# Kernel tuning notes

Hardware: AMD Instinct MI355X
Metric: run time of the kernel (lower is better)

The kernel has to match this reference:

```python
import jax, jax.numpy as jnp
import numpy as np

WINDOW = 512
STEP = 256
N_FREQ = 256
EPS = 1e-8


def setup_inputs() -> dict:
    key = jax.random.key(0)
    k1, k2, k3 = jax.random.split(key, 3)
    audio = jax.random.normal(k1, (512, 32768), dtype=jnp.float32)
    basis_real = jax.random.normal(k2, (N_FREQ, WINDOW), dtype=jnp.float32)
    basis_imag = jax.random.normal(k3, (N_FREQ, WINDOW), dtype=jnp.float32)
    return {"audio": audio, "basis_real": basis_real, "basis_imag": basis_imag}


def reference(audio, basis_real, basis_imag):
    # --- framing (windowed_audio): strided unfold -> [B, n_frames, WINDOW] ---
    n_samples = audio.shape[-1]
    n_frames = (n_samples - WINDOW) // STEP + 1  # 127 for 32768 samples
    idx = jnp.arange(n_frames)[:, None] * STEP + jnp.arange(WINDOW)[None, :]
    windowed = audio[:, idx]  # [B, F, W]

    # --- per-frame L2 normalization ---
    norms = jnp.linalg.norm(windowed, axis=-1, keepdims=True)  # [B, F, 1]
    wn = windowed / (norms + EPS)

    # --- basis normalization by complex L2 norm over window dim ---
    bnorm = jnp.sqrt(jnp.sum(basis_real * basis_real + basis_imag * basis_imag,
                             axis=-1, keepdims=True))  # [K, 1]
    br = basis_real / (bnorm + EPS)
    bi = basis_imag / (bnorm + EPS)

    # --- projection: windowed @ basis.T, real and imag parts ---
    real = jnp.einsum('bfw,kw->bfk', wn, br)  # [B, F, K]
    imag = jnp.einsum('bfw,kw->bfk', wn, bi)  # [B, F, K]
    return norms, real, imag
```

## Files before the change

### kernel.cpp

```cpp
#include <hip/hip_runtime.h>

#define WINDOW   512
#define STEPSZ   256
#define NFRAMES  127
#define NSAMP    32768
#define NBATCH   512
#define NFREQ    256
#define BM       64
#define SAMP_TILE 16640
#define NPS      65

typedef __attribute__((ext_vector_type(8)))  short short8;
typedef __attribute__((ext_vector_type(16))) float f32x16;
typedef __attribute__((ext_vector_type(4)))  float f4;

#define SWZ(byt) ((byt) ^ ((((byt) >> 9) & 7) << 4))

static __device__ __forceinline__ short f2bf(float x) {
    union { float f; unsigned u; } v; v.f = x;
    unsigned r = (v.u + 0x7fffu + ((v.u >> 16) & 1u)) >> 16;
    return (short)r;
}

__global__ __launch_bounds__(256) void prep_kernel(const float* __restrict__ br,
                                                   const float* __restrict__ bi,
                                                   short* __restrict__ Bf) {
    const int lane = threadIdx.x & 63;
    const int wid  = threadIdx.x >> 6;
    const int n    = blockIdx.x * 4 + wid;
    const float* pr = br + (size_t)n * WINDOW + lane * 8;
    const float* pi = bi + (size_t)n * WINDOW + lane * 8;
    f4 r0 = *(const f4*)pr;
    f4 r1 = *(const f4*)(pr + 4);
    f4 i0 = *(const f4*)pi;
    f4 i1 = *(const f4*)(pi + 4);
    float ss = 0.f;
#pragma unroll
    for (int j = 0; j < 4; ++j)
        ss += r0[j]*r0[j] + r1[j]*r1[j] + i0[j]*i0[j] + i1[j]*i1[j];
#pragma unroll
    for (int d = 1; d < 64; d <<= 1) ss += __shfl_xor(ss, d, 64);
    const float inv = 1.0f / (sqrtf(ss) + 1e-8f);
    short8 hr, hi;
#pragma unroll
    for (int j = 0; j < 4; ++j) {
        hr[j]     = f2bf(r0[j] * inv);
        hr[j + 4] = f2bf(r1[j] * inv);
        hi[j]     = f2bf(i0[j] * inv);
        hi[j + 4] = f2bf(i1[j] * inv);
    }
    const int ks  = lane >> 1, kg2 = lane & 1;
    const int nsR = n >> 5;
    const int nsI = 8 + (n >> 5);
    const int sl  = (n & 31) + 32 * kg2;
    *(short8*)(Bf + ((size_t)(nsR * 32 + ks) * 64 + sl) * 8) = hr;
    *(short8*)(Bf + ((size_t)(nsI * 32 + ks) * 64 + sl) * 8) = hi;
}

__global__ __launch_bounds__(512, 4) void mel_kernel(const float* __restrict__ audio,
                                                     const short* __restrict__ Bf,
                                                     float* __restrict__ out) {
    __shared__ short smp[SAMP_TILE];
    __shared__ float ps[NPS];
    __shared__ float invn[BM];

    const int tid  = threadIdx.x;
    const int lane = tid & 63;
    const int wid  = tid >> 6;

    const int b  = blockIdx.x >> 1;
    const int mh = blockIdx.x & 1;
    const int f0 = mh * BM;

    float* out_norms = out;
    float* out_real  = out + 65024;
    float* out_imag  = out + 65024 + 16646144;

    const float* abase = audio + (size_t)b * NSAMP + f0 * STEPSZ;
    const int smax = NSAMP - f0 * STEPSZ - 8;

    const int rl32 = lane & 31;
    const int kg2  = lane >> 5;
    const int wn   = wid;

    const short* bp0 = Bf + ((size_t)(2 * wn + 0) * 32 * 64 + lane) * 8;
    const short* bp1 = Bf + ((size_t)(2 * wn + 1) * 32 * 64 + lane) * 8;

    short8 bb[3][2];
#pragma unroll
    for (int d = 0; d < 3; ++d) {
        bb[d][0] = *(const short8*)(bp0 + (size_t)d * 512);
        bb[d][1] = *(const short8*)(bp1 + (size_t)d * 512);
    }

#pragma unroll
    for (int it = 0; it < 5; ++it) {
        const int sl = it * 4096 + tid * 8;
        float ss = 0.f;
        if (sl < SAMP_TILE) {
            const int slc = sl < smax ? sl : smax;
            f4 v0 = *(const f4*)(abase + slc);
            f4 v1 = *(const f4*)(abase + slc + 4);
            short8 h;
#pragma unroll
            for (int q = 0; q < 4; ++q) {
                ss += v0[q]*v0[q] + v1[q]*v1[q];
                h[q]     = f2bf(v0[q]);
                h[q + 4] = f2bf(v1[q]);
            }
            const int byt = sl * 2;
            *(short8*)((char*)smp + SWZ(byt)) = h;
        }
        ss += __shfl_xor(ss, 1, 64);
        ss += __shfl_xor(ss, 2, 64);
        ss += __shfl_xor(ss, 4, 64);
        ss += __shfl_xor(ss, 8, 64);
        ss += __shfl_xor(ss, 16, 64);
        const int chunk = (it * 4096 + tid * 8) >> 8;
        if ((tid & 31) == 0 && chunk < NPS) ps[chunk] = ss;
    }
    __syncthreads();

    if (tid < BM) {
        const float nrm = sqrtf(ps[tid] + ps[tid + 1]);
        const int fr = f0 + tid;
        if (fr < NFRAMES) out_norms[b * NFRAMES + fr] = nrm;
        invn[tid] = 1.0f / (nrm + 1e-8f);
    }

    const int rb0 = (0 * 32 + rl32) * 512 + kg2 * 16;
    const int rb1 = (1 * 32 + rl32) * 512 + kg2 * 16;
    const int X0  = (rl32 & 7) << 4;
    const int X1  = ((rl32 + 1) & 7) << 4;
    const char* sb = (const char*)smp;

    f32x16 acc[2][2];
    acc[0][0] = (f32x16)0.f; acc[0][1] = (f32x16)0.f;
    acc[1][0] = (f32x16)0.f; acc[1][1] = (f32x16)0.f;

#pragma unroll
    for (int ks = 0; ks < 32; ++ks) {
        const int X  = (ks < 16) ? X0 : X1;
        const int kb = ks * 32;
        short8 a0 = *(const short8*)(sb + ((rb0 + kb) ^ X));
        short8 a1 = *(const short8*)(sb + ((rb1 + kb) ^ X));
        const int cur = ks % 3;
        short8 cb0 = bb[cur][0];
        short8 cb1 = bb[cur][1];
        if (ks < 29) {
            bb[cur][0] = *(const short8*)(bp0 + (size_t)(ks + 3) * 512);
            bb[cur][1] = *(const short8*)(bp1 + (size_t)(ks + 3) * 512);
        }
        acc[0][0] = __builtin_amdgcn_mfma_f32_32x32x16_bf16(a0, cb0, acc[0][0], 0, 0, 0);
        acc[1][0] = __builtin_amdgcn_mfma_f32_32x32x16_bf16(a1, cb0, acc[1][0], 0, 0, 0);
        acc[0][1] = __builtin_amdgcn_mfma_f32_32x32x16_bf16(a0, cb1, acc[0][1], 0, 0, 0);
        acc[1][1] = __builtin_amdgcn_mfma_f32_32x32x16_bf16(a1, cb1, acc[1][1], 0, 0, 0);
    }
    __syncthreads();

#pragma unroll
    for (int mi = 0; mi < 2; ++mi) {
#pragma unroll
        for (int s = 0; s < 2; ++s) {
            const int n = (2 * wn + s) * 32 + rl32;
            float* dst = (n < NFREQ) ? out_real : out_imag;
            const int kcol = n & (NFREQ - 1);
            const int rbase = mi * 32 + 4 * kg2;
#pragma unroll
            for (int r = 0; r < 16; ++r) {
                const int rr = rbase + (r & 3) + 8 * (r >> 2);
                const int fr = f0 + rr;
                if (fr < NFRAMES)
                    dst[((size_t)b * NFRAMES + fr) * NFREQ + kcol] = acc[mi][s][r] * invn[rr];
            }
        }
    }
}

extern "C" void kernel_launch(void* const* d_in, const int* in_sizes, int n_in,
                              void* d_out, int out_size, void* d_ws, size_t ws_size,
                              hipStream_t stream) {
    const float* audio = (const float*)d_in[0];
    const float* br    = (const float*)d_in[1];
    const float* bi    = (const float*)d_in[2];
    float* out = (float*)d_out;
    short* Bf  = (short*)d_ws;

    prep_kernel<<<64, 256, 0, stream>>>(br, bi, Bf);
    mel_kernel<<<NBATCH * 2, 512, 0, stream>>>(audio, Bf, out);
}
```

Before: 63.16 us.

## Process both frame halves per block with double-buffered LDS staging overlapped with MFMA

Each block now handles a whole batch row, covering both 64-frame halves instead of one. While the MFMA loop runs on the first half, the audio for the second half is loaded, converted to bf16 and written into a second LDS buffer. The basis prefetch changes from a 3-deep ring to an even/odd 2-deep scheme. This hides global-load latency behind compute, but it halves the grid to 512 blocks and doubles LDS per block, which can cut occupancy and parallelism.

```diff
diff --git a/kernel.cpp b/kernel.cpp
--- a/kernel.cpp
+++ b/kernel.cpp
@@ -57,121 +57,185 @@
     *(short8*)(Bf + ((size_t)(nsI * 32 + ks) * 64 + sl) * 8) = hi;
 }
 
+#define STAGE_ISSUE(IT)                                                   \
+    if (!last) {                                                          \
+        const int sl = (IT) * 4096 + tid * 8;                             \
+        if (sl < SAMP_TILE) {                                             \
+            const int slc = sl < smax_n ? sl : smax_n;                    \
+            sv0 = *(const f4*)(abase_n + slc);                            \
+            sv1 = *(const f4*)(abase_n + slc + 4);                        \
+        }                                                                 \
+    }
+
+#define STAGE_USE(IT)                                                     \
+    if (!last) {                                                          \
+        const int sl = (IT) * 4096 + tid * 8;                             \
+        float ss = 0.f;                                                   \
+        if (sl < SAMP_TILE) {                                             \
+            short8 h;                                                     \
+            _Pragma("unroll")                                             \
+            for (int q = 0; q < 4; ++q) {                                 \
+                ss += sv0[q]*sv0[q] + sv1[q]*sv1[q];                      \
+                h[q]     = f2bf(sv0[q]);                                  \
+                h[q + 4] = f2bf(sv1[q]);                                  \
+            }                                                             \
+            *(short8*)((char*)smp[s1] + SWZ(sl * 2)) = h;                 \
+        }                                                                 \
+        ss += __shfl_xor(ss, 1, 64);                                      \
+        ss += __shfl_xor(ss, 2, 64);                                      \
+        ss += __shfl_xor(ss, 4, 64);                                      \
+        ss += __shfl_xor(ss, 8, 64);                                      \
+        ss += __shfl_xor(ss, 16, 64);                                     \
+        const int chunk = ((IT) * 4096 + tid * 8) >> 8;                   \
+        if ((tid & 31) == 0 && chunk < NPS) ps[s1][chunk] = ss;           \
+    }
+
 __global__ __launch_bounds__(512, 4) void mel_kernel(const float* __restrict__ audio,
                                                      const short* __restrict__ Bf,
                                                      float* __restrict__ out) {
-    __shared__ short smp[SAMP_TILE];
-    __shared__ float ps[NPS];
-    __shared__ float invn[BM];
+    __shared__ short smp[2][SAMP_TILE];
+    __shared__ float ps[2][NPS];
+    __shared__ float invn[2][BM];
 
     const int tid  = threadIdx.x;
     const int lane = tid & 63;
     const int wid  = tid >> 6;
 
-    const int b  = blockIdx.x >> 1;
-    const int mh = blockIdx.x & 1;
-    const int f0 = mh * BM;
+    const int b = blockIdx.x;
 
     float* out_norms = out;
     float* out_real  = out + 65024;
     float* out_imag  = out + 65024 + 16646144;
 
-    const float* abase = audio + (size_t)b * NSAMP + f0 * STEPSZ;
-    const int smax = NSAMP - f0 * STEPSZ - 8;
-
     const int rl32 = lane & 31;
     const int kg2  = lane >> 5;
     const int wn   = wid;
 
     const short* bp0 = Bf + ((size_t)(2 * wn + 0) * 32 * 64 + lane) * 8;
     const short* bp1 = Bf + ((size_t)(2 * wn + 1) * 32 * 64 + lane) * 8;
-
-    short8 bb[3][2];
-#pragma unroll
-    for (int d = 0; d < 3; ++d) {
-        bb[d][0] = *(const short8*)(bp0 + (size_t)d * 512);
-        bb[d][1] = *(const short8*)(bp1 + (size_t)d * 512);
-    }
-
-#pragma unroll
-    for (int it = 0; it < 5; ++it) {
-        const int sl = it * 4096 + tid * 8;
-        float ss = 0.f;
-        if (sl < SAMP_TILE) {
-            const int slc = sl < smax ? sl : smax;
-            f4 v0 = *(const f4*)(abase + slc);
-            f4 v1 = *(const f4*)(abase + slc + 4);
-            short8 h;
-#pragma unroll
-            for (int q = 0; q < 4; ++q) {
-                ss += v0[q]*v0[q] + v1[q]*v1[q];
-                h[q]     = f2bf(v0[q]);
-                h[q + 4] = f2bf(v1[q]);
-            }
-            const int byt = sl * 2;
-            *(short8*)((char*)smp + SWZ(byt)) = h;
-        }
-        ss += __shfl_xor(ss, 1, 64);
-        ss += __shfl_xor(ss, 2, 64);
-        ss += __shfl_xor(ss, 4, 64);
-        ss += __shfl_xor(ss, 8, 64);
-        ss += __shfl_xor(ss, 16, 64);
-        const int chunk = (it * 4096 + tid * 8) >> 8;
-        if ((tid & 31) == 0 && chunk < NPS) ps[chunk] = ss;
-    }
-    __syncthreads();
-
-    if (tid < BM) {
-        const float nrm = sqrtf(ps[tid] + ps[tid + 1]);
-        const int fr = f0 + tid;
-        if (fr < NFRAMES) out_norms[b * NFRAMES + fr] = nrm;
-        invn[tid] = 1.0f / (nrm + 1e-8f);
-    }
 
     const int rb0 = (0 * 32 + rl32) * 512 + kg2 * 16;
     const int rb1 = (1 * 32 + rl32) * 512 + kg2 * 16;
     const int X0  = (rl32 & 7) << 4;
     const int X1  = ((rl32 + 1) & 7) << 4;
-    const char* sb = (const char*)smp;
-
-    f32x16 acc[2][2];
-    acc[0][0] = (f32x16)0.f; acc[0][1] = (f32x16)0.f;
-    acc[1][0] = (f32x16)0.f; acc[1][1] = (f32x16)0.f;
-
-#pragma unroll
-    for (int ks = 0; ks < 32; ++ks) {
-        const int X  = (ks < 16) ? X0 : X1;
-        const int kb = ks * 32;
-        short8 a0 = *(const short8*)(sb + ((rb0 + kb) ^ X));
-        short8 a1 = *(const short8*)(sb + ((rb1 + kb) ^ X));
-        const int cur = ks % 3;
-        short8 cb0 = bb[cur][0];
-        short8 cb1 = bb[cur][1];
-        if (ks < 29) {
-            bb[cur][0] = *(const short8*)(bp0 + (size_t)(ks + 3) * 512);
-            bb[cur][1] = *(const short8*)(bp1 + (size_t)(ks + 3) * 512);
-        }
-        acc[0][0] = __builtin_amdgcn_mfma_f32_32x32x16_bf16(a0, cb0, acc[0][0], 0, 0, 0);
-        acc[1][0] = __builtin_amdgcn_mfma_f32_32x32x16_bf16(a1, cb0, acc[1][0], 0, 0, 0);
-        acc[0][1] = __builtin_amdgcn_mfma_f32_32x32x16_bf16(a0, cb1, acc[0][1], 0, 0, 0);
-        acc[1][1] = __builtin_amdgcn_mfma_f32_32x32x16_bf16(a1, cb1, acc[1][1], 0, 0, 0);
-    }
-    __syncthreads();
-
-#pragma unroll
-    for (int mi = 0; mi < 2; ++mi) {
-#pragma unroll
-        for (int s = 0; s < 2; ++s) {
-            const int n = (2 * wn + s) * 32 + rl32;
-            float* dst = (n < NFREQ) ? out_real : out_imag;
-            const int kcol = n & (NFREQ - 1);
-            const int rbase = mi * 32 + 4 * kg2;
-#pragma unroll
-            for (int r = 0; r < 16; ++r) {
-                const int rr = rbase + (r & 3) + 8 * (r >> 2);
-                const int fr = f0 + rr;
-                if (fr < NFRAMES)
-                    dst[((size_t)b * NFRAMES + fr) * NFREQ + kcol] = acc[mi][s][r] * invn[rr];
+
+    {
+        const float* abase = audio + (size_t)b * NSAMP;
+        const int smax = NSAMP - 8;
+#pragma unroll
+        for (int it = 0; it < 5; ++it) {
+            const int sl = it * 4096 + tid * 8;
+            float ss = 0.f;
+            if (sl < SAMP_TILE) {
+                const int slc = sl < smax ? sl : smax;
+                f4 v0 = *(const f4*)(abase + slc);
+                f4 v1 = *(const f4*)(abase + slc + 4);
+                short8 h;
+#pragma unroll
+                for (int q = 0; q < 4; ++q) {
+                    ss += v0[q]*v0[q] + v1[q]*v1[q];
+                    h[q]     = f2bf(v0[q]);
+                    h[q + 4] = f2bf(v1[q]);
+                }
+                *(short8*)((char*)smp[0] + SWZ(sl * 2)) = h;
+            }
+            ss += __shfl_xor(ss, 1, 64);
+            ss += __shfl_xor(ss, 2, 64);
+            ss += __shfl_xor(ss, 4, 64);
+            ss += __shfl_xor(ss, 8, 64);
+            ss += __shfl_xor(ss, 16, 64);
+            const int chunk = (it * 4096 + tid * 8) >> 8;
+            if ((tid & 31) == 0 && chunk < NPS) ps[0][chunk] = ss;
+        }
+        __syncthreads();
+        if (tid < BM) {
+            const float nrm = sqrtf(ps[0][tid] + ps[0][tid + 1]);
+            out_norms[b * NFRAMES + tid] = nrm;
+            invn[0][tid] = 1.0f / (nrm + 1e-8f);
+        }
+    }
+
+    for (int t = 0; t < 2; ++t) {
+        const bool last = (t == 1);
+        const int  s1   = (t + 1) & 1;
+        const int  f0   = t * BM;
+        const float* abase_n = audio + (size_t)b * NSAMP + 16384;
+        const int    smax_n  = NSAMP - 16384 - 8;
+
+        const char* sb = (const char*)smp[t & 1];
+        f4 sv0, sv1;
+
+        short8 eb0 = *(const short8*)bp0;
+        short8 eb1 = *(const short8*)bp1;
+        short8 ob0 = *(const short8*)(bp0 + 512);
+        short8 ob1 = *(const short8*)(bp1 + 512);
+
+        f32x16 acc[2][2];
+        acc[0][0] = (f32x16)0.f; acc[0][1] = (f32x16)0.f;
+        acc[1][0] = (f32x16)0.f; acc[1][1] = (f32x16)0.f;
+
+#pragma unroll
+        for (int ks = 0; ks < 32; ++ks) {
+            const int X  = (ks < 16) ? X0 : X1;
+            const int kb = ks * 32;
+            short8 a0 = *(const short8*)(sb + ((rb0 + kb) ^ X));
+            short8 a1 = *(const short8*)(sb + ((rb1 + kb) ^ X));
+
+            if (ks == 0)  { STAGE_ISSUE(0) }
+            if (ks == 4)  { STAGE_USE(0) }
+            if (ks == 6)  { STAGE_ISSUE(1) }
+            if (ks == 10) { STAGE_USE(1) }
+            if (ks == 12) { STAGE_ISSUE(2) }
+            if (ks == 16) { STAGE_USE(2) }
+            if (ks == 18) { STAGE_ISSUE(3) }
+            if (ks == 22) { STAGE_USE(3) }
+            if (ks == 24) { STAGE_ISSUE(4) }
+            if (ks == 28) { STAGE_USE(4) }
+
+            short8 cb0, cb1;
+            if ((ks & 1) == 0) {
+                cb0 = eb0; cb1 = eb1;
+                if (ks < 30) {
+                    eb0 = *(const short8*)(bp0 + (size_t)(ks + 2) * 512);
+                    eb1 = *(const short8*)(bp1 + (size_t)(ks + 2) * 512);
+                }
+            } else {
+                cb0 = ob0; cb1 = ob1;
+                if (ks < 30) {
+                    ob0 = *(const short8*)(bp0 + (size_t)(ks + 2) * 512);
+                    ob1 = *(const short8*)(bp1 + (size_t)(ks + 2) * 512);
+                }
+            }
+            acc[0][0] = __builtin_amdgcn_mfma_f32_32x32x16_bf16(a0, cb0, acc[0][0], 0, 0, 0);
+            acc[1][0] = __builtin_amdgcn_mfma_f32_32x32x16_bf16(a1, cb0, acc[1][0], 0, 0, 0);
+            acc[0][1] = __builtin_amdgcn_mfma_f32_32x32x16_bf16(a0, cb1, acc[0][1], 0, 0, 0);
+            acc[1][1] = __builtin_amdgcn_mfma_f32_32x32x16_bf16(a1, cb1, acc[1][1], 0, 0, 0);
+        }
+
+        __syncthreads();
+
+        if (!last && tid < BM) {
+            const float nrm = sqrtf(ps[s1][tid] + ps[s1][tid + 1]);
+            const int fr = BM + tid;
+            if (fr < NFRAMES) out_norms[b * NFRAMES + fr] = nrm;
+            invn[s1][tid] = 1.0f / (nrm + 1e-8f);
+        }
+
+#pragma unroll
+        for (int mi = 0; mi < 2; ++mi) {
+#pragma unroll
+            for (int s = 0; s < 2; ++s) {
+                const int n = (2 * wn + s) * 32 + rl32;
+                float* dst = (n < NFREQ) ? out_real : out_imag;
+                const int kcol = n & (NFREQ - 1);
+                const int rbase = mi * 32 + 4 * kg2;
+#pragma unroll
+                for (int r = 0; r < 16; ++r) {
+                    const int rr = rbase + (r & 3) + 8 * (r >> 2);
+                    const int fr = f0 + rr;
+                    if (fr < NFRAMES)
+                        dst[((size_t)b * NFRAMES + fr) * NFREQ + kcol] = acc[mi][s][r] * invn[t & 1][rr];
+                }
             }
         }
     }
@@ -187,5 +251,5 @@
     short* Bf  = (short*)d_ws;
 
     prep_kernel<<<64, 256, 0, stream>>>(br, bi, Bf);
-    mel_kernel<<<NBATCH * 2, 512, 0, stream>>>(audio, Bf, out);
-}
+    mel_kernel<<<NBATCH, 512, 0, stream>>>(audio, Bf, out);
+}
```

New measurement: 158.0 us. 150% more time.

## Split frame-norm computation into a separate kernel ahead of the GEMM

Applied to the files above, without the earlier changes.

Moves the per-frame L2 norm reduction out of the GEMM kernel into a dedicated norms kernel that writes the norms and inverse norms to a workspace buffer. The GEMM kernel then only converts audio to bf16, loads the precomputed inverse norms, and drops a trailing barrier. This shortens the GEMM prologue, but adds a kernel launch and a second full read of the audio.

```diff
diff --git a/kernel.cpp b/kernel.cpp
--- a/kernel.cpp
+++ b/kernel.cpp
@@ -57,12 +57,44 @@
     *(short8*)(Bf + ((size_t)(nsI * 32 + ks) * 64 + sl) * 8) = hi;
 }
 
-__global__ __launch_bounds__(512, 4) void mel_kernel(const float* __restrict__ audio,
-                                                     const short* __restrict__ Bf,
-                                                     float* __restrict__ out) {
+__global__ __launch_bounds__(512) void norms_kernel(const float* __restrict__ audio,
+                                                    float* __restrict__ invn_g,
+                                                    float* __restrict__ out_norms) {
+    __shared__ float ps[128];
+    const int tid = threadIdx.x;
+    const int b   = blockIdx.x;
+    const float* src = audio + (size_t)b * NSAMP;
+#pragma unroll
+    for (int it = 0; it < 8; ++it) {
+        const int s = it * 4096 + tid * 8;
+        f4 v0 = *(const f4*)(src + s);
+        f4 v1 = *(const f4*)(src + s + 4);
+        float ss = 0.f;
+#pragma unroll
+        for (int q = 0; q < 4; ++q) ss += v0[q]*v0[q] + v1[q]*v1[q];
+        ss += __shfl_xor(ss, 1, 64);
+        ss += __shfl_xor(ss, 2, 64);
+        ss += __shfl_xor(ss, 4, 64);
+        ss += __shfl_xor(ss, 8, 64);
+        ss += __shfl_xor(ss, 16, 64);
+        if ((tid & 31) == 0) ps[s >> 8] = ss;
+    }
+    __syncthreads();
+    if (tid < NFRAMES) {
+        const float nrm = sqrtf(ps[tid] + ps[tid + 1]);
+        out_norms[b * NFRAMES + tid] = nrm;
+        invn_g[b * 128 + tid] = 1.0f / (nrm + 1e-8f);
+    } else if (tid == 127) {
+        invn_g[b * 128 + 127] = 0.0f;
+    }
+}
+
+__global__ __launch_bounds__(512, 4) void gemm_kernel(const float* __restrict__ audio,
+                                                      const short* __restrict__ Bf,
+                                                      const float* __restrict__ invn_g,
+                                                      float* __restrict__ out) {
     __shared__ short smp[SAMP_TILE];
-    __shared__ float ps[NPS];
-    __shared__ float invn[BM];
+    __shared__ float invn_s[BM];
 
     const int tid  = threadIdx.x;
     const int lane = tid & 63;
@@ -72,9 +104,8 @@
     const int mh = blockIdx.x & 1;
     const int f0 = mh * BM;
 
-    float* out_norms = out;
-    float* out_real  = out + 65024;
-    float* out_imag  = out + 65024 + 16646144;
+    float* out_real = out + 65024;
+    float* out_imag = out + 65024 + 16646144;
 
     const float* abase = audio + (size_t)b * NSAMP + f0 * STEPSZ;
     const int smax = NSAMP - f0 * STEPSZ - 8;
@@ -96,7 +127,6 @@
 #pragma unroll
     for (int it = 0; it < 5; ++it) {
         const int sl = it * 4096 + tid * 8;
-        float ss = 0.f;
         if (sl < SAMP_TILE) {
             const int slc = sl < smax ? sl : smax;
             f4 v0 = *(const f4*)(abase + slc);
@@ -104,29 +134,14 @@
             short8 h;
 #pragma unroll
             for (int q = 0; q < 4; ++q) {
-                ss += v0[q]*v0[q] + v1[q]*v1[q];
                 h[q]     = f2bf(v0[q]);
                 h[q + 4] = f2bf(v1[q]);
             }
-            const int byt = sl * 2;
-            *(short8*)((char*)smp + SWZ(byt)) = h;
+            *(short8*)((char*)smp + SWZ(sl * 2)) = h;
         }
-        ss += __shfl_xor(ss, 1, 64);
-        ss += __shfl_xor(ss, 2, 64);
-        ss += __shfl_xor(ss, 4, 64);
-        ss += __shfl_xor(ss, 8, 64);
-        ss += __shfl_xor(ss, 16, 64);
-        const int chunk = (it * 4096 + tid * 8) >> 8;
-        if ((tid & 31) == 0 && chunk < NPS) ps[chunk] = ss;
-    }
+    }
+    if (tid < BM) invn_s[tid] = invn_g[b * 128 + f0 + tid];
     __syncthreads();
-
-    if (tid < BM) {
-        const float nrm = sqrtf(ps[tid] + ps[tid + 1]);
-        const int fr = f0 + tid;
-        if (fr < NFRAMES) out_norms[b * NFRAMES + fr] = nrm;
-        invn[tid] = 1.0f / (nrm + 1e-8f);
-    }
 
     const int rb0 = (0 * 32 + rl32) * 512 + kg2 * 16;
     const int rb1 = (1 * 32 + rl32) * 512 + kg2 * 16;
@@ -156,7 +171,6 @@
         acc[0][1] = __builtin_amdgcn_mfma_f32_32x32x16_bf16(a0, cb1, acc[0][1], 0, 0, 0);
         acc[1][1] = __builtin_amdgcn_mfma_f32_32x32x16_bf16(a1, cb1, acc[1][1], 0, 0, 0);
     }
-    __syncthreads();
 
 #pragma unroll
     for (int mi = 0; mi < 2; ++mi) {
@@ -171,7 +185,7 @@
                 const int rr = rbase + (r & 3) + 8 * (r >> 2);
                 const int fr = f0 + rr;
                 if (fr < NFRAMES)
-                    dst[((size_t)b * NFRAMES + fr) * NFREQ + kcol] = acc[mi][s][r] * invn[rr];
+                    dst[((size_t)b * NFRAMES + fr) * NFREQ + kcol] = acc[mi][s][r] * invn_s[rr];
             }
         }
     }
@@ -184,8 +198,10 @@
     const float* br    = (const float*)d_in[1];
     const float* bi    = (const float*)d_in[2];
     float* out = (float*)d_out;
-    short* Bf  = (short*)d_ws;
+    short* Bf     = (short*)d_ws;
+    float* invn_g = (float*)((char*)d_ws + (1 << 20));
 
     prep_kernel<<<64, 256, 0, stream>>>(br, bi, Bf);
-    mel_kernel<<<NBATCH * 2, 512, 0, stream>>>(audio, Bf, out);
-}
+    norms_kernel<<<NBATCH, 512, 0, stream>>>(audio, invn_g, out);
+    gemm_kernel<<<NBATCH * 2, 512, 0, stream>>>(audio, Bf, invn_g, out);
+}
```

New measurement: 73.82 us. +16.9%, slower.

## Double threads per block, giving each wave one 32-column B tile

Applied to the files above, without the earlier changes.

Blocks grow from 512 to 1024 threads (16 waves). Each wave now computes a 64x32 output tile with two accumulators instead of 64x64 with four. The audio staging loop loads 4 floats per thread and reduces the partial norms across a full 64-lane wave. The B operand prefetch changes from triple-buffering two tiles to double-buffering one, and a barrier is added so invn is ready before the epilogue. The aim is more waves for latency hiding and fewer registers per wave, at the cost of more redundant A-fragment LDS reads per MFMA and possible limits on block residency.

```diff
diff --git a/kernel.cpp b/kernel.cpp
--- a/kernel.cpp
+++ b/kernel.cpp
@@ -11,6 +11,7 @@
 #define NPS      65
 
 typedef __attribute__((ext_vector_type(8)))  short short8;
+typedef __attribute__((ext_vector_type(4)))  short bf16x4v;
 typedef __attribute__((ext_vector_type(16))) float f32x16;
 typedef __attribute__((ext_vector_type(4)))  float f4;
 
@@ -57,9 +58,9 @@
     *(short8*)(Bf + ((size_t)(nsI * 32 + ks) * 64 + sl) * 8) = hi;
 }
 
-__global__ __launch_bounds__(512, 4) void mel_kernel(const float* __restrict__ audio,
-                                                     const short* __restrict__ Bf,
-                                                     float* __restrict__ out) {
+__global__ __launch_bounds__(1024, 8) void mel_kernel(const float* __restrict__ audio,
+                                                      const short* __restrict__ Bf,
+                                                      float* __restrict__ out) {
     __shared__ short smp[SAMP_TILE];
     __shared__ float ps[NPS];
     __shared__ float invn[BM];
@@ -77,47 +78,34 @@
     float* out_imag  = out + 65024 + 16646144;
 
     const float* abase = audio + (size_t)b * NSAMP + f0 * STEPSZ;
-    const int smax = NSAMP - f0 * STEPSZ - 8;
+    const int smax = NSAMP - f0 * STEPSZ - 4;
 
     const int rl32 = lane & 31;
     const int kg2  = lane >> 5;
-    const int wn   = wid;
-
-    const short* bp0 = Bf + ((size_t)(2 * wn + 0) * 32 * 64 + lane) * 8;
-    const short* bp1 = Bf + ((size_t)(2 * wn + 1) * 32 * 64 + lane) * 8;
-
-    short8 bb[3][2];
-#pragma unroll
-    for (int d = 0; d < 3; ++d) {
-        bb[d][0] = *(const short8*)(bp0 + (size_t)d * 512);
-        bb[d][1] = *(const short8*)(bp1 + (size_t)d * 512);
-    }
 
 #pragma unroll
     for (int it = 0; it < 5; ++it) {
-        const int sl = it * 4096 + tid * 8;
+        const int sl = it * 4096 + tid * 4;
         float ss = 0.f;
         if (sl < SAMP_TILE) {
             const int slc = sl < smax ? sl : smax;
-            f4 v0 = *(const f4*)(abase + slc);
-            f4 v1 = *(const f4*)(abase + slc + 4);
-            short8 h;
+            f4 v = *(const f4*)(abase + slc);
+            bf16x4v h;
 #pragma unroll
             for (int q = 0; q < 4; ++q) {
-                ss += v0[q]*v0[q] + v1[q]*v1[q];
-                h[q]     = f2bf(v0[q]);
-                h[q + 4] = f2bf(v1[q]);
+                ss += v[q] * v[q];
+                h[q] = f2bf(v[q]);
             }
-            const int byt = sl * 2;
-            *(short8*)((char*)smp + SWZ(byt)) = h;
+            *(bf16x4v*)((char*)smp + SWZ(sl * 2)) = h;
         }
         ss += __shfl_xor(ss, 1, 64);
         ss += __shfl_xor(ss, 2, 64);
         ss += __shfl_xor(ss, 4, 64);
         ss += __shfl_xor(ss, 8, 64);
         ss += __shfl_xor(ss, 16, 64);
-        const int chunk = (it * 4096 + tid * 8) >> 8;
-        if ((tid & 31) == 0 && chunk < NPS) ps[chunk] = ss;
+        ss += __shfl_xor(ss, 32, 64);
+        const int chunk = (it * 4096 + tid * 4) >> 8;
+        if ((tid & 63) == 0 && chunk < NPS) ps[chunk] = ss;
     }
     __syncthreads();
 
@@ -127,6 +115,7 @@
         if (fr < NFRAMES) out_norms[b * NFRAMES + fr] = nrm;
         invn[tid] = 1.0f / (nrm + 1e-8f);
     }
+    __syncthreads();
 
     const int rb0 = (0 * 32 + rl32) * 512 + kg2 * 16;
     const int rb1 = (1 * 32 + rl32) * 512 + kg2 * 16;
@@ -134,9 +123,13 @@
     const int X1  = ((rl32 + 1) & 7) << 4;
     const char* sb = (const char*)smp;
 
-    f32x16 acc[2][2];
-    acc[0][0] = (f32x16)0.f; acc[0][1] = (f32x16)0.f;
-    acc[1][0] = (f32x16)0.f; acc[1][1] = (f32x16)0.f;
+    const short* bp = Bf + ((size_t)wid * 32 * 64 + lane) * 8;
+
+    short8 eb = *(const short8*)bp;
+    short8 ob = *(const short8*)(bp + 512);
+
+    f32x16 acc0 = (f32x16)0.f;
+    f32x16 acc1 = (f32x16)0.f;
 
 #pragma unroll
     for (int ks = 0; ks < 32; ++ks) {
@@ -144,35 +137,31 @@
         const int kb = ks * 32;
         short8 a0 = *(const short8*)(sb + ((rb0 + kb) ^ X));
         short8 a1 = *(const short8*)(sb + ((rb1 + kb) ^ X));
-        const int cur = ks % 3;
-        short8 cb0 = bb[cur][0];
-        short8 cb1 = bb[cur][1];
-        if (ks < 29) {
-            bb[cur][0] = *(const short8*)(bp0 + (size_t)(ks + 3) * 512);
-            bb[cur][1] = *(const short8*)(bp1 + (size_t)(ks + 3) * 512);
+        short8 cb;
+        if ((ks & 1) == 0) {
+            cb = eb;
+            if (ks < 30) eb = *(const short8*)(bp + (size_t)(ks + 2) * 512);
+        } else {
+            cb = ob;
+            if (ks < 30) ob = *(const short8*)(bp + (size_t)(ks + 2) * 512);
         }
-        acc[0][0] = __builtin_amdgcn_mfma_f32_32x32x16_bf16(a0, cb0, acc[0][0], 0, 0, 0);
-        acc[1][0] = __builtin_amdgcn_mfma_f32_32x32x16_bf16(a1, cb0, acc[1][0], 0, 0, 0);
-        acc[0][1] = __builtin_amdgcn_mfma_f32_32x32x16_bf16(a0, cb1, acc[0][1], 0, 0, 0);
-        acc[1][1] = __builtin_amdgcn_mfma_f32_32x32x16_bf16(a1, cb1, acc[1][1], 0, 0, 0);
+        acc0 = __builtin_amdgcn_mfma_f32_32x32x16_bf16(a0, cb, acc0, 0, 0, 0);
+        acc1 = __builtin_amdgcn_mfma_f32_32x32x16_bf16(a1, cb, acc1, 0, 0, 0);
     }
-    __syncthreads();
 
+    const int n    = wid * 32 + rl32;
+    float* dst     = (n < NFREQ) ? out_real : out_imag;
+    const int kcol = n & (NFREQ - 1);
 #pragma unroll
     for (int mi = 0; mi < 2; ++mi) {
+        const f32x16 a = mi ? acc1 : acc0;
+        const int rbase = mi * 32 + 4 * kg2;
 #pragma unroll
-        for (int s = 0; s < 2; ++s) {
-            const int n = (2 * wn + s) * 32 + rl32;
-            float* dst = (n < NFREQ) ? out_real : out_imag;
-            const int kcol = n & (NFREQ - 1);
-            const int rbase = mi * 32 + 4 * kg2;
-#pragma unroll
-            for (int r = 0; r < 16; ++r) {
-                const int rr = rbase + (r & 3) + 8 * (r >> 2);
-                const int fr = f0 + rr;
-                if (fr < NFRAMES)
-                    dst[((size_t)b * NFRAMES + fr) * NFREQ + kcol] = acc[mi][s][r] * invn[rr];
-            }
+        for (int r = 0; r < 16; ++r) {
+            const int rr = rbase + (r & 3) + 8 * (r >> 2);
+            const int fr = f0 + rr;
+            if (fr < NFRAMES)
+                dst[((size_t)b * NFRAMES + fr) * NFREQ + kcol] = a[r] * invn[rr];
         }
     }
 }
@@ -187,5 +176,5 @@
     short* Bf  = (short*)d_ws;
 
     prep_kernel<<<64, 256, 0, stream>>>(br, bi, Bf);
-    mel_kernel<<<NBATCH * 2, 512, 0, stream>>>(audio, Bf, out);
+    mel_kernel<<<NBATCH * 2, 1024, 0, stream>>>(audio, Bf, out);
 }
```

Measured after the change: 125.4 us. 98.5% more time.
